# Optimization experiments

Hardware: AMD Instinct MI355X
Metric: run time of the kernel (lower is better)

The kernel has to match this reference:

```python
import jax, jax.numpy as jnp
import numpy as np

# Multi-scale deformable attention (MSDeformableAttention from RTDETRTransformerv2)
SPATIAL = ((80, 80), (40, 40), (20, 20))  # (h, w) per level, strides 8/16/32 on 640x640
N_HEADS, N_LEVELS, N_POINTS = 8, 3, 4
D_MODEL = 256
HEAD_DIM = D_MODEL // N_HEADS


def setup_inputs() -> dict:
    key = jax.random.key(0)
    ks = jax.random.split(key, 10)
    B, Q = 16, 300
    Lv = sum(h * w for h, w in SPATIAL)  # 8400
    s = 0.02
    return {
        "query": jax.random.normal(ks[0], (B, Q, D_MODEL), jnp.float32),
        "reference_points": jax.random.uniform(ks[1], (B, Q, 4), jnp.float32),
        "value": jax.random.normal(ks[2], (B, Lv, D_MODEL), jnp.float32),
        "Wv": jax.random.normal(ks[3], (D_MODEL, D_MODEL), jnp.float32) * s,
        "bv": jnp.zeros((D_MODEL,), jnp.float32),
        "Woff": jax.random.normal(ks[4], (D_MODEL, N_HEADS * N_LEVELS * N_POINTS * 2), jnp.float32) * s,
        "boff": jax.random.normal(ks[5], (N_HEADS * N_LEVELS * N_POINTS * 2,), jnp.float32) * 0.1,
        "Wattn": jax.random.normal(ks[6], (D_MODEL, N_HEADS * N_LEVELS * N_POINTS), jnp.float32) * s,
        "battn": jnp.zeros((N_HEADS * N_LEVELS * N_POINTS,), jnp.float32),
        "Wout": jax.random.normal(ks[7], (D_MODEL, D_MODEL), jnp.float32) * s,
        "bout": jnp.zeros((D_MODEL,), jnp.float32),
    }


def _grid_sample_level(v_lvl, gx, gy, h, w):
    """Bilinear grid_sample, align_corners=False, zeros padding.

    v_lvl : (B, nH, h*w, hd) flattened per-level value map
    gx,gy : (B, nH, P) sample coords in [-1, 1]
    returns (B, nH, P, hd)
    """
    px = ((gx + 1.0) * w - 1.0) * 0.5  # pixel x
    py = ((gy + 1.0) * h - 1.0) * 0.5  # pixel y
    x0 = jnp.floor(px)
    y0 = jnp.floor(py)
    fx = px - x0
    fy = py - y0
    x0i = x0.astype(jnp.int32)
    y0i = y0.astype(jnp.int32)

    def corner(xi, yi, wgt):
        valid = (xi >= 0) & (xi < w) & (yi >= 0) & (yi < h)
        idx = jnp.clip(yi, 0, h - 1) * w + jnp.clip(xi, 0, w - 1)
        g = jnp.take_along_axis(v_lvl, idx[..., None], axis=2)  # (B,nH,P,hd)
        return g * (wgt * valid.astype(wgt.dtype))[..., None]

    return (corner(x0i, y0i, (1 - fx) * (1 - fy))
            + corner(x0i + 1, y0i, fx * (1 - fy))
            + corner(x0i, y0i + 1, (1 - fx) * fy)
            + corner(x0i + 1, y0i + 1, fx * fy))


def reference(query, reference_points, value, Wv, bv, Woff, boff, Wattn, battn, Wout, bout):
    B, Q, _ = query.shape
    # value projection -> per-head values
    v = (value @ Wv + bv).reshape(B, -1, N_HEADS, HEAD_DIM)
    # sampling offsets and attention weights from queries
    off = (query @ Woff + boff).reshape(B, Q, N_HEADS, N_LEVELS, N_POINTS, 2)
    aw = jax.nn.softmax(
        (query @ Wattn + battn).reshape(B, Q, N_HEADS, N_LEVELS * N_POINTS), axis=-1
    ).reshape(B, Q, N_HEADS, N_LEVELS, N_POINTS)
    # reference points (cx, cy) broadcast over heads/levels/points
    ref = reference_points[:, :, None, None, None, :2]
    pts = jnp.clip(ref + off, 0.0, 1.0)      # (B,Q,nH,nL,nP,2) in [0,1]
    g = pts * 2.0 - 1.0                      # grid_sample coords in [-1,1]

    out = jnp.zeros((B, Q, N_HEADS, HEAD_DIM), query.dtype)
    start = 0
    for lvl, (h, w) in enumerate(SPATIAL):
        v_lvl = v[:, start:start + h * w].transpose(0, 2, 1, 3)  # (B,nH,hw,hd)
        gl = g[:, :, :, lvl]                                     # (B,Q,nH,nP,2)
        gx = gl[..., 0].transpose(0, 2, 1, 3).reshape(B, N_HEADS, Q * N_POINTS)
        gy = gl[..., 1].transpose(0, 2, 1, 3).reshape(B, N_HEADS, Q * N_POINTS)
        sampled = _grid_sample_level(v_lvl, gx, gy, h, w)        # (B,nH,Q*nP,hd)
        sampled = sampled.reshape(B, N_HEADS, Q, N_POINTS, HEAD_DIM)
        wl = aw[:, :, :, lvl].transpose(0, 2, 1, 3)              # (B,nH,Q,nP)
        out = out + jnp.einsum('bhqpd,bhqp->bqhd', sampled, wl)
        start += h * w

    return out.reshape(B, Q, D_MODEL) @ Wout + bout
```

## Files before the change

### kernel.cpp

```cpp
#include <hip/hip_runtime.h>
#include <hip/hip_bf16.h>
#include <cstddef>

#define NB 16
#define NQ 300
#define DM 256
#define LV_ 8400

typedef __attribute__((ext_vector_type(8))) short short8;
typedef __attribute__((ext_vector_type(4))) float f32x4;

static __device__ __forceinline__ unsigned short bf16_rne(float f) {
  unsigned int u = __builtin_bit_cast(unsigned int, f);
  u += 0x7FFFu + ((u >> 16) & 1u);
  return (unsigned short)(u >> 16);
}

static __device__ __forceinline__ unsigned int pack_bf2(float a, float b) {
  __hip_bfloat162 p = __float22bfloat162_rn(make_float2(a, b));
  unsigned int u;
  __builtin_memcpy(&u, &p, 4);
  return u;
}

__global__ void wconv_kernel(const float* __restrict__ W,
                             unsigned short* __restrict__ Wth) {
  const int n = blockIdx.x, k = threadIdx.x;
  Wth[n * DM + k] = bf16_rne(W[k * DM + n]);
}

__global__ __launch_bounds__(256) void vproj_mfma(
    const float* __restrict__ A, const unsigned short* __restrict__ Wth,
    const float* __restrict__ bias, unsigned short* __restrict__ V) {
  __shared__ short Ah[4][128][8];
  __shared__ short Bh[4][128][8];
  const int tid = threadIdx.x;
  const int lane = tid & 63;
  const int wave = tid >> 6;
  const int l16 = lane & 15, q4 = lane >> 4;
  const int wr = (wave >> 1) * 64, wc = (wave & 1) * 64;
  const size_t row0 = (size_t)blockIdx.x * 128;
  const int col0 = blockIdx.y * 128;

  const int arow = tid >> 1;
  const int half = tid & 1;
  const int c0 = half * 2;

  f32x4 acc[4][4];
  #pragma unroll
  for (int i = 0; i < 4; ++i)
    #pragma unroll
    for (int j = 0; j < 4; ++j) acc[i][j] = (f32x4)0.f;

  const float* ap0 = A + (row0 + arow) * DM + half * 16;
  const unsigned short* wp0 = Wth + (size_t)(col0 + arow) * DM + half * 16;

  for (int kk = 0; kk < DM; kk += 32) {
    const float4 f0 = *(const float4*)(ap0 + kk + 0);
    const float4 f1 = *(const float4*)(ap0 + kk + 4);
    const float4 f2 = *(const float4*)(ap0 + kk + 8);
    const float4 f3 = *(const float4*)(ap0 + kk + 12);
    const uint4 w0 = *(const uint4*)(wp0 + kk);
    const uint4 w1 = *(const uint4*)(wp0 + kk + 8);
    uint4 p0, p1;
    p0.x = pack_bf2(f0.x, f0.y); p0.y = pack_bf2(f0.z, f0.w);
    p0.z = pack_bf2(f1.x, f1.y); p0.w = pack_bf2(f1.z, f1.w);
    p1.x = pack_bf2(f2.x, f2.y); p1.y = pack_bf2(f2.z, f2.w);
    p1.z = pack_bf2(f3.x, f3.y); p1.w = pack_bf2(f3.z, f3.w);
    __syncthreads();
    *(uint4*)&Ah[c0][arow][0]     = p0;
    *(uint4*)&Ah[c0 + 1][arow][0] = p1;
    *(uint4*)&Bh[c0][arow][0]     = w0;
    *(uint4*)&Bh[c0 + 1][arow][0] = w1;
    __syncthreads();

    short8 af[4], bfr[4];
    #pragma unroll
    for (int i = 0; i < 4; ++i)
      af[i] = *(const short8*)&Ah[q4][wr + i * 16 + l16][0];
    #pragma unroll
    for (int j = 0; j < 4; ++j)
      bfr[j] = *(const short8*)&Bh[q4][wc + j * 16 + l16][0];
    #pragma unroll
    for (int i = 0; i < 4; ++i)
      #pragma unroll
      for (int j = 0; j < 4; ++j)
        acc[i][j] = __builtin_amdgcn_mfma_f32_16x16x32_bf16(af[i], bfr[j], acc[i][j], 0, 0, 0);
  }

  #pragma unroll
  for (int i = 0; i < 4; ++i)
    #pragma unroll
    for (int j = 0; j < 4; ++j) {
      const int col = col0 + wc + j * 16 + l16;
      const float bcol = bias[col];
      #pragma unroll
      for (int r = 0; r < 4; ++r) {
        const size_t row = row0 + wr + i * 16 + q4 * 4 + r;
        V[row * DM + col] = bf16_rne(acc[i][j][r] + bcol);
      }
    }
}

__global__ __launch_bounds__(256) void gemm64(
    const float* __restrict__ A, const float* __restrict__ W,
    const float* __restrict__ bias, float* __restrict__ C,
    int M, int N, int K) {
  __shared__ float As[16][64];
  __shared__ float Bs[16][64];
  const int tid = threadIdx.x;
  const int tx = tid & 15, ty = tid >> 4;
  const int m0 = blockIdx.x * 64, n0 = blockIdx.y * 64;
  const int ar = tid & 63, ak4 = (tid >> 6) * 4;
  const int bk = tid >> 4, bc4 = (tid & 15) * 4;
  const int bcol = n0 + bc4;

  float acc[4][4];
  #pragma unroll
  for (int i = 0; i < 4; ++i)
    #pragma unroll
    for (int j = 0; j < 4; ++j) acc[i][j] = 0.f;

  for (int kk = 0; kk < K; kk += 16) {
    const float4 av = *(const float4*)(A + (size_t)(m0 + ar) * K + kk + ak4);
    float4 wv = make_float4(0.f, 0.f, 0.f, 0.f);
    if (bcol < N) wv = *(const float4*)(W + (size_t)(kk + bk) * N + bcol);
    __syncthreads();
    As[ak4 + 0][ar] = av.x;
    As[ak4 + 1][ar] = av.y;
    As[ak4 + 2][ar] = av.z;
    As[ak4 + 3][ar] = av.w;
    *(float4*)&Bs[bk][bc4] = wv;
    __syncthreads();
    #pragma unroll
    for (int k = 0; k < 16; ++k) {
      const float4 a4 = *(const float4*)&As[k][ty * 4];
      const float4 b4 = *(const float4*)&Bs[k][tx * 4];
      const float* aa = (const float*)&a4;
      const float* bb = (const float*)&b4;
      #pragma unroll
      for (int i = 0; i < 4; ++i)
        #pragma unroll
        for (int j = 0; j < 4; ++j)
          acc[i][j] = fmaf(aa[i], bb[j], acc[i][j]);
    }
  }

  if (n0 + tx * 4 < N) {
    const float4 bi = *(const float4*)&bias[n0 + tx * 4];
    const float* bb = (const float*)&bi;
    #pragma unroll
    for (int i = 0; i < 4; ++i) {
      float4 o;
      o.x = acc[i][0] + bb[0];
      o.y = acc[i][1] + bb[1];
      o.z = acc[i][2] + bb[2];
      o.w = acc[i][3] + bb[3];
      *(float4*)(C + (size_t)(m0 + ty * 4 + i) * N + n0 + tx * 4) = o;
    }
  }
}

__global__ __launch_bounds__(256) void sample_kernel(
    const float* __restrict__ refp, const unsigned short* __restrict__ v,
    const float* __restrict__ off, const float* __restrict__ logits,
    float* __restrict__ mid) {
  const int bq0 = blockIdx.x * 2;
  const int b = bq0 / NQ;
  const int t = threadIdx.x;
  __shared__ float off_sh[2][192];
  __shared__ float aw_sh[2][96];
  __shared__ int   idx_sh[2][96][4];
  __shared__ float wt_sh[2][96][4];
  __shared__ float ref_sh[2][2];

  {
    const float* osrc = off + (size_t)bq0 * 192;
    float* odst = &off_sh[0][0];
    odst[t] = osrc[t];
    if (t < 128) odst[256 + t] = osrc[256 + t];
    const float* lsrc = logits + (size_t)bq0 * 96;
    if (t < 192) (&aw_sh[0][0])[t] = lsrc[t];
    if (t < 4) ref_sh[t >> 1][t & 1] = refp[(bq0 + (t >> 1)) * 4 + (t & 1)];
  }
  __syncthreads();

  if (t < 16) {
    const int q = t >> 3, h = t & 7;
    float* aw = &aw_sh[q][h * 12];
    float m = -1e30f;
    #pragma unroll
    for (int i = 0; i < 12; ++i) m = fmaxf(m, aw[i]);
    float e[12], s = 0.f;
    #pragma unroll
    for (int i = 0; i < 12; ++i) { e[i] = __expf(aw[i] - m); s += e[i]; }
    const float inv = 1.f / s;
    #pragma unroll
    for (int i = 0; i < 12; ++i) aw[i] = e[i] * inv;
  }
  __syncthreads();

  if (t < 192) {
    const int q = t / 96, r = t - q * 96;
    const int h = r / 12, lp = r - h * 12;
    const int l = lp >> 2, p = lp & 3;
    const int LH[3] = {80, 40, 20};
    const int LS[3] = {0, 6400, 8000};
    const int hh = LH[l], ww = LH[l], st = LS[l];
    const int oi = ((h * 3 + l) * 4 + p) * 2;
    const float aw = aw_sh[q][h * 12 + lp];
    const float sx = fminf(fmaxf(ref_sh[q][0] + off_sh[q][oi], 0.f), 1.f);
    const float sy = fminf(fmaxf(ref_sh[q][1] + off_sh[q][oi + 1], 0.f), 1.f);
    const float px = sx * (float)ww - 0.5f;
    const float py = sy * (float)hh - 0.5f;
    const float x0f = floorf(px), y0f = floorf(py);
    const float fx = px - x0f, fy = py - y0f;
    const int x0 = (int)x0f, y0 = (int)y0f;
    const int x1 = x0 + 1, y1 = y0 + 1;
    const bool vx0 = (x0 >= 0) & (x0 < ww), vx1 = (x1 >= 0) & (x1 < ww);
    const bool vy0 = (y0 >= 0) & (y0 < hh), vy1 = (y1 >= 0) & (y1 < hh);
    const int x0c = min(max(x0, 0), ww - 1), x1c = min(max(x1, 0), ww - 1);
    const int y0c = min(max(y0, 0), hh - 1), y1c = min(max(y1, 0), hh - 1);
    idx_sh[q][r][0] = st + y0c * ww + x0c;
    idx_sh[q][r][1] = st + y0c * ww + x1c;
    idx_sh[q][r][2] = st + y1c * ww + x0c;
    idx_sh[q][r][3] = st + y1c * ww + x1c;
    wt_sh[q][r][0] = aw * (1.f - fx) * (1.f - fy) * ((vx0 & vy0) ? 1.f : 0.f);
    wt_sh[q][r][1] = aw * fx * (1.f - fy) * ((vx1 & vy0) ? 1.f : 0.f);
    wt_sh[q][r][2] = aw * (1.f - fx) * fy * ((vx0 & vy1) ? 1.f : 0.f);
    wt_sh[q][r][3] = aw * fx * fy * ((vx1 & vy1) ? 1.f : 0.f);
  }
  __syncthreads();

  const int q = t >> 7, h = (t >> 4) & 7, dp = t & 15;
  const unsigned short* vb = v + (size_t)b * LV_ * DM + h * 32 + dp * 2;
  float ax = 0.f, ay = 0.f;
  #pragma unroll
  for (int r = 0; r < 12; ++r) {
    const int rr = h * 12 + r;
    #pragma unroll
    for (int c = 0; c < 4; ++c) {
      const int id = idx_sh[q][rr][c];
      const float w = wt_sh[q][rr][c];
      const unsigned int u = *(const unsigned int*)(vb + (size_t)id * DM);
      ax = fmaf(w, __builtin_bit_cast(float, u << 16), ax);
      ay = fmaf(w, __builtin_bit_cast(float, u & 0xFFFF0000u), ay);
    }
  }
  float2 o; o.x = ax; o.y = ay;
  *(float2*)(mid + (size_t)(bq0 + q) * DM + h * 32 + dp * 2) = o;
}

extern "C" void kernel_launch(void* const* d_in, const int* in_sizes, int n_in,
                              void* d_out, int out_size, void* d_ws, size_t ws_size,
                              hipStream_t stream) {
  (void)in_sizes; (void)n_in; (void)out_size; (void)ws_size;
  const float* query = (const float*)d_in[0];
  const float* refp  = (const float*)d_in[1];
  const float* value = (const float*)d_in[2];
  const float* Wv    = (const float*)d_in[3];
  const float* bv    = (const float*)d_in[4];
  const float* Woff  = (const float*)d_in[5];
  const float* boff  = (const float*)d_in[6];
  const float* Wattn = (const float*)d_in[7];
  const float* battn = (const float*)d_in[8];
  const float* Wout  = (const float*)d_in[9];
  const float* bout  = (const float*)d_in[10];
  float* out = (float*)d_out;

  char* ws = (char*)d_ws;
  unsigned short* v_bf = (unsigned short*)ws;
  unsigned short* Wth  = (unsigned short*)(ws + 68812800);
  float* offb   = (float*)(ws + 68943872);
  float* logitb = (float*)(ws + 72630272);
  float* midb   = (float*)(ws + 74473472);

  wconv_kernel<<<DM, DM, 0, stream>>>(Wv, Wth);
  vproj_mfma<<<dim3((NB * LV_) / 128, 2), 256, 0, stream>>>(value, Wth, bv, v_bf);
  gemm64<<<dim3(75, 3), 256, 0, stream>>>(query, Woff, boff, offb, 4800, 192, 256);
  gemm64<<<dim3(75, 2), 256, 0, stream>>>(query, Wattn, battn, logitb, 4800, 96, 256);
  sample_kernel<<<2400, 256, 0, stream>>>(refp, v_bf, offb, logitb, midb);
  gemm64<<<dim3(75, 4), 256, 0, stream>>>(midb, Wout, bout, out, 4800, 256, 256);
}
```

Baseline: 347.3 us.

## Fuse query projections, use bf16 MFMA output projection, prefetch GEMM tiles

Several changes land together. A tiled transpose kernel now converts both Wv and Wout to bf16. The offset and attention-logit GEMMs are merged into one launch with smaller 32x32 tiles and register prefetch. The value-projection MFMA loop gains software prefetch of the next K slice. The sampling kernel writes bf16 output and remaps block indices to interleave batches. The fp32 output GEMM is replaced by a bf16 MFMA kernel, which cuts launches and memory traffic at the cost of extra bf16 rounding on the intermediate.

Result: faster. 295.6 us (-14.9%).

```diff
diff --git a/kernel.cpp b/kernel.cpp
--- a/kernel.cpp
+++ b/kernel.cpp
@@ -23,10 +23,21 @@
   return u;
 }
 
-__global__ void wconv_kernel(const float* __restrict__ W,
-                             unsigned short* __restrict__ Wth) {
-  const int n = blockIdx.x, k = threadIdx.x;
-  Wth[n * DM + k] = bf16_rne(W[k * DM + n]);
+__global__ __launch_bounds__(256) void prep_kernel(
+    const float* __restrict__ Wv, const float* __restrict__ Wout,
+    unsigned short* __restrict__ Wth, unsigned short* __restrict__ WoutT) {
+  const float* src = blockIdx.z ? Wout : Wv;
+  unsigned short* dst = blockIdx.z ? WoutT : Wth;
+  __shared__ float tle[32][33];
+  const int k0 = blockIdx.x * 32, n0 = blockIdx.y * 32;
+  const int xx = threadIdx.x & 31, y4 = (threadIdx.x >> 5) * 4;
+  #pragma unroll
+  for (int i = 0; i < 4; ++i)
+    tle[y4 + i][xx] = src[(size_t)(k0 + y4 + i) * DM + n0 + xx];
+  __syncthreads();
+  #pragma unroll
+  for (int i = 0; i < 4; ++i)
+    dst[(size_t)(n0 + y4 + i) * DM + k0 + xx] = bf16_rne(tle[xx][y4 + i]);
 }
 
 __global__ __launch_bounds__(256) void vproj_mfma(
@@ -55,24 +66,35 @@
   const float* ap0 = A + (row0 + arow) * DM + half * 16;
   const unsigned short* wp0 = Wth + (size_t)(col0 + arow) * DM + half * 16;
 
+  float4 f0 = *(const float4*)(ap0 + 0);
+  float4 f1 = *(const float4*)(ap0 + 4);
+  float4 f2 = *(const float4*)(ap0 + 8);
+  float4 f3 = *(const float4*)(ap0 + 12);
+  uint4 w0 = *(const uint4*)(wp0);
+  uint4 w1 = *(const uint4*)(wp0 + 8);
+
   for (int kk = 0; kk < DM; kk += 32) {
-    const float4 f0 = *(const float4*)(ap0 + kk + 0);
-    const float4 f1 = *(const float4*)(ap0 + kk + 4);
-    const float4 f2 = *(const float4*)(ap0 + kk + 8);
-    const float4 f3 = *(const float4*)(ap0 + kk + 12);
-    const uint4 w0 = *(const uint4*)(wp0 + kk);
-    const uint4 w1 = *(const uint4*)(wp0 + kk + 8);
     uint4 p0, p1;
     p0.x = pack_bf2(f0.x, f0.y); p0.y = pack_bf2(f0.z, f0.w);
     p0.z = pack_bf2(f1.x, f1.y); p0.w = pack_bf2(f1.z, f1.w);
     p1.x = pack_bf2(f2.x, f2.y); p1.y = pack_bf2(f2.z, f2.w);
     p1.z = pack_bf2(f3.x, f3.y); p1.w = pack_bf2(f3.z, f3.w);
+    uint4 cw0 = w0, cw1 = w1;
     __syncthreads();
     *(uint4*)&Ah[c0][arow][0]     = p0;
     *(uint4*)&Ah[c0 + 1][arow][0] = p1;
-    *(uint4*)&Bh[c0][arow][0]     = w0;
-    *(uint4*)&Bh[c0 + 1][arow][0] = w1;
-    __syncthreads();
+    *(uint4*)&Bh[c0][arow][0]     = cw0;
+    *(uint4*)&Bh[c0 + 1][arow][0] = cw1;
+    __syncthreads();
+
+    if (kk + 32 < DM) {
+      f0 = *(const float4*)(ap0 + kk + 32);
+      f1 = *(const float4*)(ap0 + kk + 36);
+      f2 = *(const float4*)(ap0 + kk + 40);
+      f3 = *(const float4*)(ap0 + kk + 44);
+      w0 = *(const uint4*)(wp0 + kk + 32);
+      w1 = *(const uint4*)(wp0 + kk + 40);
+    }
 
     short8 af[4], bfr[4];
     #pragma unroll
@@ -102,71 +124,68 @@
     }
 }
 
-__global__ __launch_bounds__(256) void gemm64(
-    const float* __restrict__ A, const float* __restrict__ W,
-    const float* __restrict__ bias, float* __restrict__ C,
-    int M, int N, int K) {
-  __shared__ float As[16][64];
-  __shared__ float Bs[16][64];
+__global__ __launch_bounds__(256) void gemm_qp(
+    const float* __restrict__ q,
+    const float* __restrict__ Woff, const float* __restrict__ boff,
+    const float* __restrict__ Wattn, const float* __restrict__ battn,
+    float* __restrict__ offb, float* __restrict__ logitb) {
+  const int by = blockIdx.y;
+  const float* W; const float* bias; float* C; int N, c0;
+  if (by < 6) { W = Woff;  bias = boff;  C = offb;   N = 192; c0 = by * 32; }
+  else        { W = Wattn; bias = battn; C = logitb; N = 96;  c0 = (by - 6) * 32; }
+  const int m0 = blockIdx.x * 32;
+
+  __shared__ float As[32][33];
+  __shared__ float Bs[32][33];
   const int tid = threadIdx.x;
+  const int ar = tid >> 3, ak = (tid & 7) * 4;
+  const int kr = tid >> 3, bc = (tid & 7) * 4;
   const int tx = tid & 15, ty = tid >> 4;
-  const int m0 = blockIdx.x * 64, n0 = blockIdx.y * 64;
-  const int ar = tid & 63, ak4 = (tid >> 6) * 4;
-  const int bk = tid >> 4, bc4 = (tid & 15) * 4;
-  const int bcol = n0 + bc4;
-
-  float acc[4][4];
-  #pragma unroll
-  for (int i = 0; i < 4; ++i)
-    #pragma unroll
-    for (int j = 0; j < 4; ++j) acc[i][j] = 0.f;
-
-  for (int kk = 0; kk < K; kk += 16) {
-    const float4 av = *(const float4*)(A + (size_t)(m0 + ar) * K + kk + ak4);
-    float4 wv = make_float4(0.f, 0.f, 0.f, 0.f);
-    if (bcol < N) wv = *(const float4*)(W + (size_t)(kk + bk) * N + bcol);
-    __syncthreads();
-    As[ak4 + 0][ar] = av.x;
-    As[ak4 + 1][ar] = av.y;
-    As[ak4 + 2][ar] = av.z;
-    As[ak4 + 3][ar] = av.w;
-    *(float4*)&Bs[bk][bc4] = wv;
-    __syncthreads();
-    #pragma unroll
-    for (int k = 0; k < 16; ++k) {
-      const float4 a4 = *(const float4*)&As[k][ty * 4];
-      const float4 b4 = *(const float4*)&Bs[k][tx * 4];
-      const float* aa = (const float*)&a4;
-      const float* bb = (const float*)&b4;
-      #pragma unroll
-      for (int i = 0; i < 4; ++i)
-        #pragma unroll
-        for (int j = 0; j < 4; ++j)
-          acc[i][j] = fmaf(aa[i], bb[j], acc[i][j]);
-    }
-  }
-
-  if (n0 + tx * 4 < N) {
-    const float4 bi = *(const float4*)&bias[n0 + tx * 4];
-    const float* bb = (const float*)&bi;
-    #pragma unroll
-    for (int i = 0; i < 4; ++i) {
-      float4 o;
-      o.x = acc[i][0] + bb[0];
-      o.y = acc[i][1] + bb[1];
-      o.z = acc[i][2] + bb[2];
-      o.w = acc[i][3] + bb[3];
-      *(float4*)(C + (size_t)(m0 + ty * 4 + i) * N + n0 + tx * 4) = o;
-    }
+
+  const float* apt = q + (size_t)(m0 + ar) * DM + ak;
+  float4 av = *(const float4*)apt;
+  float4 wv = *(const float4*)(W + (size_t)kr * N + c0 + bc);
+
+  float acc[2][2] = {{0.f, 0.f}, {0.f, 0.f}};
+  for (int kk = 0; kk < DM; kk += 32) {
+    __syncthreads();
+    As[ak + 0][ar] = av.x;
+    As[ak + 1][ar] = av.y;
+    As[ak + 2][ar] = av.z;
+    As[ak + 3][ar] = av.w;
+    *(float4*)&Bs[kr][bc] = wv;
+    __syncthreads();
+    if (kk + 32 < DM) {
+      av = *(const float4*)(apt + kk + 32);
+      wv = *(const float4*)(W + (size_t)(kk + 32 + kr) * N + c0 + bc);
+    }
+    #pragma unroll
+    for (int k = 0; k < 32; ++k) {
+      const float2 a2 = *(const float2*)&As[k][ty * 2];
+      const float2 b2 = *(const float2*)&Bs[k][tx * 2];
+      acc[0][0] = fmaf(a2.x, b2.x, acc[0][0]);
+      acc[0][1] = fmaf(a2.x, b2.y, acc[0][1]);
+      acc[1][0] = fmaf(a2.y, b2.x, acc[1][0]);
+      acc[1][1] = fmaf(a2.y, b2.y, acc[1][1]);
+    }
+  }
+  const float b0 = bias[c0 + tx * 2], b1 = bias[c0 + tx * 2 + 1];
+  #pragma unroll
+  for (int i = 0; i < 2; ++i) {
+    float2 o; o.x = acc[i][0] + b0; o.y = acc[i][1] + b1;
+    *(float2*)&C[(size_t)(m0 + ty * 2 + i) * N + c0 + tx * 2] = o;
   }
 }
 
 __global__ __launch_bounds__(256) void sample_kernel(
     const float* __restrict__ refp, const unsigned short* __restrict__ v,
     const float* __restrict__ off, const float* __restrict__ logits,
-    float* __restrict__ mid) {
-  const int bq0 = blockIdx.x * 2;
-  const int b = bq0 / NQ;
+    unsigned short* __restrict__ mid) {
+  const int x = blockIdx.x;
+  const int c8 = x & 7, kb = x >> 3;
+  const int b = c8 + (kb >= 150 ? 8 : 0);
+  const int qp = (kb >= 150 ? kb - 150 : kb);
+  const int bq0 = b * NQ + qp * 2;
   const int t = threadIdx.x;
   __shared__ float off_sh[2][192];
   __shared__ float aw_sh[2][96];
@@ -239,16 +258,64 @@
   for (int r = 0; r < 12; ++r) {
     const int rr = h * 12 + r;
     #pragma unroll
-    for (int c = 0; c < 4; ++c) {
-      const int id = idx_sh[q][rr][c];
-      const float w = wt_sh[q][rr][c];
+    for (int cc = 0; cc < 4; ++cc) {
+      const int id = idx_sh[q][rr][cc];
+      const float w = wt_sh[q][rr][cc];
       const unsigned int u = *(const unsigned int*)(vb + (size_t)id * DM);
       ax = fmaf(w, __builtin_bit_cast(float, u << 16), ax);
       ay = fmaf(w, __builtin_bit_cast(float, u & 0xFFFF0000u), ay);
     }
   }
-  float2 o; o.x = ax; o.y = ay;
-  *(float2*)(mid + (size_t)(bq0 + q) * DM + h * 32 + dp * 2) = o;
+  unsigned short* mp = mid + (size_t)(bq0 + q) * DM + h * 32 + dp * 2;
+  *(unsigned int*)mp = pack_bf2(ax, ay);
+}
+
+__global__ __launch_bounds__(256) void outp_mfma(
+    const unsigned short* __restrict__ midb, const unsigned short* __restrict__ WoutT,
+    const float* __restrict__ bias, float* __restrict__ out) {
+  __shared__ short Ah[4][64][8];
+  __shared__ short Bh[4][64][8];
+  const int tid = threadIdx.x;
+  const int lane = tid & 63;
+  const int wave = tid >> 6;
+  const int l16 = lane & 15, q4 = lane >> 4;
+  const int wc = wave * 16;
+  const int m0 = blockIdx.x * 64, col0 = blockIdx.y * 64;
+
+  const int r = tid >> 2, ch = tid & 3;
+  const unsigned short* apt = midb + (size_t)(m0 + r) * DM + ch * 8;
+  const unsigned short* wpt = WoutT + (size_t)(col0 + r) * DM + ch * 8;
+  uint4 am = *(const uint4*)apt;
+  uint4 wm = *(const uint4*)wpt;
+
+  f32x4 acc[4];
+  #pragma unroll
+  for (int i = 0; i < 4; ++i) acc[i] = (f32x4)0.f;
+
+  for (int kk = 0; kk < DM; kk += 32) {
+    __syncthreads();
+    *(uint4*)&Ah[ch][r][0] = am;
+    *(uint4*)&Bh[ch][r][0] = wm;
+    __syncthreads();
+    if (kk + 32 < DM) {
+      am = *(const uint4*)(apt + kk + 32);
+      wm = *(const uint4*)(wpt + kk + 32);
+    }
+    const short8 bfrag = *(const short8*)&Bh[q4][wc + l16][0];
+    #pragma unroll
+    for (int i = 0; i < 4; ++i) {
+      const short8 af = *(const short8*)&Ah[q4][i * 16 + l16][0];
+      acc[i] = __builtin_amdgcn_mfma_f32_16x16x32_bf16(af, bfrag, acc[i], 0, 0, 0);
+    }
+  }
+
+  const int col = col0 + wc + l16;
+  const float bcol = bias[col];
+  #pragma unroll
+  for (int i = 0; i < 4; ++i)
+    #pragma unroll
+    for (int rr = 0; rr < 4; ++rr)
+      out[(size_t)(m0 + i * 16 + q4 * 4 + rr) * DM + col] = acc[i][rr] + bcol;
 }
 
 extern "C" void kernel_launch(void* const* d_in, const int* in_sizes, int n_in,
@@ -269,16 +336,16 @@
   float* out = (float*)d_out;
 
   char* ws = (char*)d_ws;
-  unsigned short* v_bf = (unsigned short*)ws;
-  unsigned short* Wth  = (unsigned short*)(ws + 68812800);
-  float* offb   = (float*)(ws + 68943872);
-  float* logitb = (float*)(ws + 72630272);
-  float* midb   = (float*)(ws + 74473472);
-
-  wconv_kernel<<<DM, DM, 0, stream>>>(Wv, Wth);
+  unsigned short* v_bf  = (unsigned short*)ws;
+  unsigned short* Wth   = (unsigned short*)(ws + 68812800);
+  unsigned short* WoutT = (unsigned short*)(ws + 68943872);
+  float* offb   = (float*)(ws + 69074944);
+  float* logitb = (float*)(ws + 72761344);
+  unsigned short* midb = (unsigned short*)(ws + 74604544);
+
+  prep_kernel<<<dim3(8, 8, 2), 256, 0, stream>>>(Wv, Wout, Wth, WoutT);
+  gemm_qp<<<dim3(150, 9), 256, 0, stream>>>(query, Woff, boff, Wattn, battn, offb, logitb);
   vproj_mfma<<<dim3((NB * LV_) / 128, 2), 256, 0, stream>>>(value, Wth, bv, v_bf);
-  gemm64<<<dim3(75, 3), 256, 0, stream>>>(query, Woff, boff, offb, 4800, 192, 256);
-  gemm64<<<dim3(75, 2), 256, 0, stream>>>(query, Wattn, battn, logitb, 4800, 96, 256);
   sample_kernel<<<2400, 256, 0, stream>>>(refp, v_bf, offb, logitb, midb);
-  gemm64<<<dim3(75, 4), 256, 0, stream>>>(midb, Wout, bout, out, 4800, 256, 256);
-}
+  outp_mfma<<<dim3(75, 4), 256, 0, stream>>>(midb, WoutT, bout, out);
+}
```
